# Performance work log

Measured on AMD Instinct MI355X. Metric: run time of the kernel, lower is better.

## Reference

```python
import jax, jax.numpy as jnp
import numpy as np
import math

D_MODEL = 512
SLOPE = 0.5  # slope_init, not trainable


def setup_inputs() -> dict:
    key = jax.random.key(0)
    k1, k2, k3, k4 = jax.random.split(key, 4)
    B, S, D = 4, 4096, D_MODEL
    x = jax.random.normal(k1, (B, S, D), dtype=jnp.float32)
    # nn.Linear(d, d): weight is [d, d]; query_key weight used as x @ W (no transpose, bias unused)
    lim = 1.0 / math.sqrt(D)
    W_qk = jax.random.uniform(k2, (D, D), jnp.float32, -lim, lim)
    W_v = jax.random.uniform(k3, (D, D), jnp.float32, -lim, lim)
    b_v = jax.random.uniform(k4, (D,), jnp.float32, -lim, lim)
    return {"x": x, "W_qk": W_qk, "W_v": W_v, "b_v": b_v}


def reference(x, W_qk, W_v, b_v):
    B, S, D = x.shape
    scale = 1.0 / math.sqrt(D)
    # scores[b,i,j] = (x @ W_qk @ x^T) * scale   (torch: x @ weight @ x.transpose)
    scores = jnp.einsum('bid,de,bje->bij', x, W_qk, x) * scale
    # ALiBi bias: (j - i) * slope
    i = jnp.arange(S, dtype=x.dtype)[:, None]
    j = jnp.arange(S, dtype=x.dtype)[None, :]
    scores = scores + (j - i) * jnp.asarray(SLOPE, x.dtype)
    # causal mask: strict upper triangle -> -inf
    causal = j > i  # [S, S] bool
    scores = jnp.where(causal, -jnp.inf, scores)
    attn = jax.nn.softmax(scores, axis=-1)
    # value_linear: x @ W_v^T + b_v (standard nn.Linear)
    v = jnp.einsum('bjd,ed->bje', x, W_v) + b_v
    return jnp.einsum('bij,bje->bie', attn, v)
```

## Files before the change

kernel.cpp:

```cpp
#include <hip/hip_runtime.h>
#include <math.h>

#define D_MODEL 512
#define SEQ     4096
#define BATCH   4
#define BS      (BATCH * SEQ)

typedef __attribute__((ext_vector_type(8))) short  short8;
typedef __attribute__((ext_vector_type(4))) float  float4v;

#define GAS __attribute__((address_space(1)))
#define LAS __attribute__((address_space(3)))

__device__ __forceinline__ void gld_lds16(const void* g, void* l) {
  __builtin_amdgcn_global_load_lds((const GAS unsigned int*)g,
                                   (LAS unsigned int*)l, 16, 0, 0);
}

__device__ __forceinline__ unsigned short bf16r(float f) {
  unsigned int u = __builtin_bit_cast(unsigned int, f);
  u += 0x7fffu + ((u >> 16) & 1u);
  return (unsigned short)(u >> 16);
}

__device__ __forceinline__ uint4 pack8(float4 a, float4 b) {
  uint4 o;
  o.x = bf16r(a.x) | ((unsigned)bf16r(a.y) << 16);
  o.y = bf16r(a.z) | ((unsigned)bf16r(a.w) << 16);
  o.z = bf16r(b.x) | ((unsigned)bf16r(b.y) << 16);
  o.w = bf16r(b.z) | ((unsigned)bf16r(b.w) << 16);
  return o;
}

__global__ __launch_bounds__(256) void cvt_w(const float* __restrict__ Wqk,
                                             unsigned short* __restrict__ Wqkt,
                                             const float* __restrict__ Wv,
                                             unsigned short* __restrict__ Wvb) {
  if (blockIdx.x < 64) {
    __shared__ float tile[64][65];
    const int bx = blockIdx.x & 7;
    const int by = blockIdx.x >> 3;
    const int tx = threadIdx.x & 63;
    const int ty = threadIdx.x >> 6;
    for (int r = ty; r < 64; r += 4)
      tile[r][tx] = Wqk[(size_t)(by * 64 + r) * D_MODEL + bx * 64 + tx];
    __syncthreads();
    for (int r = ty; r < 64; r += 4)
      Wqkt[(size_t)(bx * 64 + r) * D_MODEL + by * 64 + tx] = bf16r(tile[tx][r]);
  } else {
    const int idx = ((blockIdx.x - 64) * 256 + threadIdx.x) * 8;
    const float4 a = *(const float4*)(Wv + idx);
    const float4 b = *(const float4*)(Wv + idx + 4);
    *(uint4*)(Wvb + idx) = pack8(a, b);
  }
}

template <bool VT>
__device__ __forceinline__ void gemm_path(const float* __restrict__ x,
                                          const unsigned short* __restrict__ Wgt,
                                          const float* __restrict__ bias,
                                          unsigned short* __restrict__ xb,
                                          unsigned short* __restrict__ C,
                                          int a0, float alpha,
                                          unsigned short* Ws, unsigned short* As) {
  const int t    = threadIdx.x;
  const int w    = t >> 6;
  const int lane = t & 63;
  const int q    = lane >> 4;
  const int c    = lane & 15;
  const int wbase = w * 128;

  const int arow = t >> 2;
  const int acb  = (t & 3) * 16;

  constexpr int NI = VT ? 8 : 4;
  constexpr int NJ = VT ? 4 : 8;

  float4v acc[NI][NJ];
#pragma unroll
  for (int i = 0; i < NI; ++i)
#pragma unroll
    for (int j = 0; j < NJ; ++j) acc[i][j] = (float4v){0.f, 0.f, 0.f, 0.f};

  for (int k0 = 0; k0 < D_MODEL; k0 += 64) {
#pragma unroll
    for (int it = 0; it < 16; ++it) {
      const int idx = it * 256 + t;
      gld_lds16(Wgt + (size_t)(idx >> 3) * D_MODEL + k0 + (idx & 7) * 8,
                &Ws[idx * 8]);
    }
    {
      const float* xg = x + (size_t)(a0 + arow) * D_MODEL + k0 + acb;
      const float4 f0 = *(const float4*)(xg + 0);
      const float4 f1 = *(const float4*)(xg + 4);
      const float4 f2 = *(const float4*)(xg + 8);
      const float4 f3 = *(const float4*)(xg + 12);
      const uint4 u0 = pack8(f0, f1);
      const uint4 u1 = pack8(f2, f3);
      *(uint4*)&As[arow * 64 + acb]     = u0;
      *(uint4*)&As[arow * 64 + acb + 8] = u1;
      if (!VT) {
        unsigned short* xo = xb + (size_t)(a0 + arow) * D_MODEL + k0 + acb;
        *(uint4*)xo       = u0;
        *(uint4*)(xo + 8) = u1;
      }
    }
    __syncthreads();

#pragma unroll
    for (int kc = 0; kc < 2; ++kc) {
      short8 af[NI], bf[NJ];
#pragma unroll
      for (int i = 0; i < NI; ++i) {
        const unsigned short* src = VT ? &Ws[(wbase + i * 16 + c) * 64 + kc * 32 + q * 8]
                                       : &As[(i * 16 + c) * 64 + kc * 32 + q * 8];
        af[i] = *(const short8*)src;
      }
#pragma unroll
      for (int j = 0; j < NJ; ++j) {
        const unsigned short* src = VT ? &As[(j * 16 + c) * 64 + kc * 32 + q * 8]
                                       : &Ws[(wbase + j * 16 + c) * 64 + kc * 32 + q * 8];
        bf[j] = *(const short8*)src;
      }
#pragma unroll
      for (int i = 0; i < NI; ++i)
#pragma unroll
        for (int j = 0; j < NJ; ++j)
          acc[i][j] = __builtin_amdgcn_mfma_f32_16x16x32_bf16(af[i], bf[j], acc[i][j], 0, 0, 0);
    }
    __syncthreads();
  }

  if (!VT) {
#pragma unroll
    for (int i = 0; i < NI; ++i)
#pragma unroll
      for (int tt = 0; tt < 4; ++tt) {
        const int row = a0 + i * 16 + 4 * q + tt;
#pragma unroll
        for (int j = 0; j < NJ; ++j)
          C[(size_t)row * D_MODEL + wbase + j * 16 + c] = bf16r(alpha * acc[i][j][tt]);
      }
  } else {
#pragma unroll
    for (int i = 0; i < NI; ++i)
#pragma unroll
      for (int tt = 0; tt < 4; ++tt) {
        const int dim = wbase + i * 16 + 4 * q + tt;
        const float bv = bias[dim];
#pragma unroll
        for (int j = 0; j < NJ; ++j)
          C[(size_t)dim * BS + a0 + j * 16 + c] = bf16r(acc[i][j][tt] + bv);
      }
  }
}

__global__ __launch_bounds__(256, 2) void qv_gemm(const float* __restrict__ x,
                                                  const unsigned short* __restrict__ Wqkt,
                                                  const unsigned short* __restrict__ Wvb,
                                                  const float* __restrict__ bv,
                                                  unsigned short* __restrict__ xb,
                                                  unsigned short* __restrict__ Qb,
                                                  unsigned short* __restrict__ Vt,
                                                  float scale) {
  __shared__ unsigned short Ws[512 * 64];
  __shared__ unsigned short As[64 * 64];
  if (blockIdx.x < 256)
    gemm_path<false>(x, Wqkt, nullptr, xb, Qb, blockIdx.x * 64, scale, Ws, As);
  else
    gemm_path<true>(x, Wvb, bv, nullptr, Vt, (blockIdx.x - 256) * 64, 1.0f, Ws, As);
}

__global__ __launch_bounds__(128) void attn_tile(const unsigned short* __restrict__ Q,
                                                 const unsigned short* __restrict__ Kx,
                                                 const unsigned short* __restrict__ Vt,
                                                 float* __restrict__ out) {
  constexpr int PLD = 72;
  __shared__ unsigned short pls[16 * PLD];
  __shared__ float lm[2][16], ls[2][16];

  const int t    = threadIdx.x;
  const int h    = t >> 6;
  const int lane = t & 63;
  const int q    = lane >> 4;
  const int c    = lane & 15;

  const int tile = ((blockIdx.x & 7) << 7) + (blockIdx.x >> 3);
  const int r0   = tile << 4;
  const int b    = r0 >> 12;
  const int i0   = r0 & (SEQ - 1);
  const int jb   = i0 - 48;

  short8 qf[16];
  {
    const unsigned short* qp = Q + (size_t)(r0 + c) * D_MODEL + q * 8;
#pragma unroll
    for (int ch = 0; ch < 16; ++ch) qf[ch] = *(const short8*)(qp + ch * 32);
  }

  float4v sacc[2];
  sacc[0] = (float4v){0.f, 0.f, 0.f, 0.f};
  sacc[1] = (float4v){0.f, 0.f, 0.f, 0.f};
#pragma unroll
  for (int s = 0; s < 2; ++s) {
    const int sj = 2 * h + s;
    if (jb + 16 * sj + 15 < 0) continue;
    int krow = jb + 16 * sj + c;
    if (krow < 0) krow = 0;
    const unsigned short* kr = Kx + ((size_t)(b << 12) + krow) * D_MODEL + q * 8;
    float4v sv = sacc[s];
#pragma unroll
    for (int ch = 0; ch < 16; ++ch)
      sv = __builtin_amdgcn_mfma_f32_16x16x32_bf16(qf[ch], *(const short8*)(kr + ch * 32), sv, 0, 0, 0);
    sacc[s] = sv;
  }

  float tmax[4] = {-1e30f, -1e30f, -1e30f, -1e30f};
#pragma unroll
  for (int s = 0; s < 2; ++s)
#pragma unroll
    for (int tt = 0; tt < 4; ++tt) {
      const int jl = jb + 16 * (2 * h + s) + c;
      const int il = i0 + 4 * q + tt;
      float sv = sacc[s][tt];
      sv = (jl < 0 || jl > il) ? -1e30f : sv + 0.5f * (float)(jl - il);
      sacc[s][tt] = sv;
      tmax[tt] = fmaxf(tmax[tt], sv);
    }
#pragma unroll
  for (int tt = 0; tt < 4; ++tt) {
    float v = tmax[tt];
    v = fmaxf(v, __shfl_xor(v, 1, 64));
    v = fmaxf(v, __shfl_xor(v, 2, 64));
    v = fmaxf(v, __shfl_xor(v, 4, 64));
    v = fmaxf(v, __shfl_xor(v, 8, 64));
    tmax[tt] = v;
  }
  if (c == 0) {
#pragma unroll
    for (int tt = 0; tt < 4; ++tt) lm[h][4 * q + tt] = tmax[tt];
  }
  __syncthreads();

  float m[4];
#pragma unroll
  for (int tt = 0; tt < 4; ++tt)
    m[tt] = fmaxf(lm[0][4 * q + tt], lm[1][4 * q + tt]);

  float rsum[4] = {0.f, 0.f, 0.f, 0.f};
#pragma unroll
  for (int s = 0; s < 2; ++s)
#pragma unroll
    for (int tt = 0; tt < 4; ++tt) {
      const float p = __expf(sacc[s][tt] - m[tt]);
      rsum[tt] += p;
      pls[(4 * q + tt) * PLD + (2 * h + s) * 16 + c] = bf16r(p);
    }
#pragma unroll
  for (int tt = 0; tt < 4; ++tt) {
    float v = rsum[tt];
    v += __shfl_xor(v, 1, 64);
    v += __shfl_xor(v, 2, 64);
    v += __shfl_xor(v, 4, 64);
    v += __shfl_xor(v, 8, 64);
    rsum[tt] = v;
  }
  if (c == 0) {
#pragma unroll
    for (int tt = 0; tt < 4; ++tt) ls[h][4 * q + tt] = rsum[tt];
  }
  __syncthreads();

  float l[4];
#pragma unroll
  for (int tt = 0; tt < 4; ++tt)
    l[tt] = ls[0][4 * q + tt] + ls[1][4 * q + tt];

  float4v oacc[16];
#pragma unroll
  for (int dt = 0; dt < 16; ++dt) oacc[dt] = (float4v){0.f, 0.f, 0.f, 0.f};

#pragma unroll
  for (int c2 = 0; c2 < 2; ++c2) {
    if (jb + 32 * c2 + 31 < 0) continue;
    const short8 pa = *(const short8*)&pls[c * PLD + c2 * 32 + q * 8];
    int kk = jb + c2 * 32 + q * 8;
    if (kk < 0) kk = 0;
    const unsigned short* vb = Vt + (size_t)(h * 256 + c) * BS + (b << 12) + kk;
#pragma unroll
    for (int dt = 0; dt < 16; ++dt) {
      const short8 vf = *(const short8*)(vb + (size_t)dt * 16 * BS);
      oacc[dt] = __builtin_amdgcn_mfma_f32_16x16x32_bf16(pa, vf, oacc[dt], 0, 0, 0);
    }
  }

  float inv[4];
#pragma unroll
  for (int tt = 0; tt < 4; ++tt) inv[tt] = 1.0f / l[tt];
#pragma unroll
  for (int dt = 0; dt < 16; ++dt)
#pragma unroll
    for (int tt = 0; tt < 4; ++tt)
      out[(size_t)(r0 + 4 * q + tt) * D_MODEL + h * 256 + dt * 16 + c] =
          oacc[dt][tt] * inv[tt];
}

extern "C" void kernel_launch(void* const* d_in, const int* in_sizes, int n_in,
                              void* d_out, int out_size, void* d_ws,
                              size_t ws_size, hipStream_t stream) {
  const float* x   = (const float*)d_in[0];
  const float* Wqk = (const float*)d_in[1];
  const float* Wv  = (const float*)d_in[2];
  const float* bv  = (const float*)d_in[3];
  float* out = (float*)d_out;

  unsigned short* xb   = (unsigned short*)d_ws;
  unsigned short* Qb   = xb + (size_t)BS * D_MODEL;
  unsigned short* Vt   = Qb + (size_t)BS * D_MODEL;
  unsigned short* Wqkt = Vt + (size_t)BS * D_MODEL;
  unsigned short* Wvb  = Wqkt + (size_t)D_MODEL * D_MODEL;

  const float scale = 1.0f / sqrtf((float)D_MODEL);

  cvt_w<<<dim3(192), dim3(256), 0, stream>>>(Wqk, Wqkt, Wv, Wvb);
  qv_gemm<<<dim3(512), dim3(256), 0, stream>>>(x, Wqkt, Wvb, bv, xb, Qb, Vt, scale);
  attn_tile<<<dim3(BS / 16), dim3(128), 0, stream>>>(Qb, xb, Vt, out);
}
```

Baseline: 140.5 us.

## Pre-convert x to bf16 in cvt kernel and prefetch V fragments early

The fp32-to-bf16 conversion of x moves out of the GEMM into the weight-conversion kernel. The GEMM then loads its A tile with direct global-to-LDS loads, the same way it loads weights, instead of converting in registers. In the attention kernel, the first chunk of V fragments is loaded right after the QK MFMAs so the load latency overlaps the softmax. This cuts the GEMM's register-path fp32 reads (x was read twice, once per GEMM path), at the cost of an extra pass over x and more live registers in the attention kernel.

```diff
diff --git a/kernel.cpp b/kernel.cpp
--- a/kernel.cpp
+++ b/kernel.cpp
@@ -35,7 +35,9 @@
 __global__ __launch_bounds__(256) void cvt_w(const float* __restrict__ Wqk,
                                              unsigned short* __restrict__ Wqkt,
                                              const float* __restrict__ Wv,
-                                             unsigned short* __restrict__ Wvb) {
+                                             unsigned short* __restrict__ Wvb,
+                                             const float* __restrict__ x,
+                                             unsigned short* __restrict__ xb) {
   if (blockIdx.x < 64) {
     __shared__ float tile[64][65];
     const int bx = blockIdx.x & 7;
@@ -47,19 +49,23 @@
     __syncthreads();
     for (int r = ty; r < 64; r += 4)
       Wqkt[(size_t)(bx * 64 + r) * D_MODEL + by * 64 + tx] = bf16r(tile[tx][r]);
-  } else {
+  } else if (blockIdx.x < 192) {
     const int idx = ((blockIdx.x - 64) * 256 + threadIdx.x) * 8;
     const float4 a = *(const float4*)(Wv + idx);
     const float4 b = *(const float4*)(Wv + idx + 4);
     *(uint4*)(Wvb + idx) = pack8(a, b);
+  } else {
+    const size_t idx = ((size_t)(blockIdx.x - 192) * 256 + threadIdx.x) * 8;
+    const float4 a = *(const float4*)(x + idx);
+    const float4 b = *(const float4*)(x + idx + 4);
+    *(uint4*)(xb + idx) = pack8(a, b);
   }
 }
 
 template <bool VT>
-__device__ __forceinline__ void gemm_path(const float* __restrict__ x,
+__device__ __forceinline__ void gemm_path(const unsigned short* __restrict__ xb,
                                           const unsigned short* __restrict__ Wgt,
                                           const float* __restrict__ bias,
-                                          unsigned short* __restrict__ xb,
                                           unsigned short* __restrict__ C,
                                           int a0, float alpha,
                                           unsigned short* Ws, unsigned short* As) {
@@ -70,9 +76,6 @@
   const int c    = lane & 15;
   const int wbase = w * 128;
 
-  const int arow = t >> 2;
-  const int acb  = (t & 3) * 16;
-
   constexpr int NI = VT ? 8 : 4;
   constexpr int NJ = VT ? 4 : 8;
 
@@ -89,21 +92,11 @@
       gld_lds16(Wgt + (size_t)(idx >> 3) * D_MODEL + k0 + (idx & 7) * 8,
                 &Ws[idx * 8]);
     }
-    {
-      const float* xg = x + (size_t)(a0 + arow) * D_MODEL + k0 + acb;
-      const float4 f0 = *(const float4*)(xg + 0);
-      const float4 f1 = *(const float4*)(xg + 4);
-      const float4 f2 = *(const float4*)(xg + 8);
-      const float4 f3 = *(const float4*)(xg + 12);
-      const uint4 u0 = pack8(f0, f1);
-      const uint4 u1 = pack8(f2, f3);
-      *(uint4*)&As[arow * 64 + acb]     = u0;
-      *(uint4*)&As[arow * 64 + acb + 8] = u1;
-      if (!VT) {
-        unsigned short* xo = xb + (size_t)(a0 + arow) * D_MODEL + k0 + acb;
-        *(uint4*)xo       = u0;
-        *(uint4*)(xo + 8) = u1;
-      }
+#pragma unroll
+    for (int it = 0; it < 2; ++it) {
+      const int idx = it * 256 + t;
+      gld_lds16(xb + (size_t)(a0 + (idx >> 3)) * D_MODEL + k0 + (idx & 7) * 8,
+                &As[idx * 8]);
     }
     __syncthreads();
 
@@ -155,20 +148,19 @@
   }
 }
 
-__global__ __launch_bounds__(256, 2) void qv_gemm(const float* __restrict__ x,
+__global__ __launch_bounds__(256, 2) void qv_gemm(const unsigned short* __restrict__ xb,
                                                   const unsigned short* __restrict__ Wqkt,
                                                   const unsigned short* __restrict__ Wvb,
                                                   const float* __restrict__ bv,
-                                                  unsigned short* __restrict__ xb,
                                                   unsigned short* __restrict__ Qb,
                                                   unsigned short* __restrict__ Vt,
                                                   float scale) {
   __shared__ unsigned short Ws[512 * 64];
   __shared__ unsigned short As[64 * 64];
   if (blockIdx.x < 256)
-    gemm_path<false>(x, Wqkt, nullptr, xb, Qb, blockIdx.x * 64, scale, Ws, As);
+    gemm_path<false>(xb, Wqkt, nullptr, Qb, blockIdx.x * 64, scale, Ws, As);
   else
-    gemm_path<true>(x, Wvb, bv, nullptr, Vt, (blockIdx.x - 256) * 64, 1.0f, Ws, As);
+    gemm_path<true>(xb, Wvb, bv, Vt, (blockIdx.x - 256) * 64, 1.0f, Ws, As);
 }
 
 __global__ __launch_bounds__(128) void attn_tile(const unsigned short* __restrict__ Q,
@@ -215,6 +207,17 @@
     sacc[s] = sv;
   }
 
+  const unsigned short* vbase = Vt + (size_t)(h * 256 + c) * BS + (b << 12);
+  const bool ch0 = (jb + 31 >= 0);
+  short8 vf0[16];
+  if (ch0) {
+    int kk = jb + q * 8;
+    if (kk < 0) kk = 0;
+    const unsigned short* vb = vbase + kk;
+#pragma unroll
+    for (int dt = 0; dt < 16; ++dt) vf0[dt] = *(const short8*)(vb + (size_t)dt * 16 * BS);
+  }
+
   float tmax[4] = {-1e30f, -1e30f, -1e30f, -1e30f};
 #pragma unroll
   for (int s = 0; s < 2; ++s)
@@ -280,13 +283,17 @@
 #pragma unroll
   for (int dt = 0; dt < 16; ++dt) oacc[dt] = (float4v){0.f, 0.f, 0.f, 0.f};
 
-#pragma unroll
-  for (int c2 = 0; c2 < 2; ++c2) {
-    if (jb + 32 * c2 + 31 < 0) continue;
-    const short8 pa = *(const short8*)&pls[c * PLD + c2 * 32 + q * 8];
-    int kk = jb + c2 * 32 + q * 8;
+  if (ch0) {
+    const short8 pa = *(const short8*)&pls[c * PLD + q * 8];
+#pragma unroll
+    for (int dt = 0; dt < 16; ++dt)
+      oacc[dt] = __builtin_amdgcn_mfma_f32_16x16x32_bf16(pa, vf0[dt], oacc[dt], 0, 0, 0);
+  }
+  {
+    const short8 pa = *(const short8*)&pls[c * PLD + 32 + q * 8];
+    int kk = jb + 32 + q * 8;
     if (kk < 0) kk = 0;
-    const unsigned short* vb = Vt + (size_t)(h * 256 + c) * BS + (b << 12) + kk;
+    const unsigned short* vb = vbase + kk;
 #pragma unroll
     for (int dt = 0; dt < 16; ++dt) {
       const short8 vf = *(const short8*)(vb + (size_t)dt * 16 * BS);
@@ -322,7 +329,7 @@
 
   const float scale = 1.0f / sqrtf((float)D_MODEL);
 
-  cvt_w<<<dim3(192), dim3(256), 0, stream>>>(Wqk, Wqkt, Wv, Wvb);
-  qv_gemm<<<dim3(512), dim3(256), 0, stream>>>(x, Wqkt, Wvb, bv, xb, Qb, Vt, scale);
+  cvt_w<<<dim3(192 + (BS * D_MODEL / 2048)), dim3(256), 0, stream>>>(Wqk, Wqkt, Wv, Wvb, x, xb);
+  qv_gemm<<<dim3(512), dim3(256), 0, stream>>>(xb, Wqkt, Wvb, bv, Qb, Vt, scale);
   attn_tile<<<dim3(BS / 16), dim3(128), 0, stream>>>(Qb, xb, Vt, out);
 }
```

After: 135.7 us. 1.04x faster.
